# Optimization experiments

Hardware: AMD Instinct MI355X
Metric: run time of the kernel (lower is better)

Reference implementation:

```python
import jax, jax.numpy as jnp
import numpy as np

VOCAB, ATTR, B = 50257, 16, 256
EMB, ATTR_EMB, HID, ZDIM = 300, 200, 700, 500
MAXLEN = 30
SOS_IDX, EOS_IDX = 1, 2


def setup_inputs() -> dict:
    ks = jax.random.split(jax.random.key(0), 8)
    s = 0.02
    return {
        "z": jax.random.normal(ks[0], (B, ZDIM), jnp.float32),
        "l": jax.random.randint(ks[1], (B,), 0, ATTR),
        "emb_w": jax.random.normal(ks[2], (VOCAB, EMB), jnp.float32) * s,
        "attr_w": jax.random.normal(ks[3], (ATTR, ATTR_EMB), jnp.float32) * s,
        "W_ih": jax.random.normal(ks[4], (3 * HID, EMB), jnp.float32) * s,
        "W_hh": jax.random.normal(ks[5], (3 * HID, HID), jnp.float32) * s,
        "b_ih": jnp.zeros((3 * HID,), jnp.float32),
        "b_hh": jnp.zeros((3 * HID,), jnp.float32),
        "out_w": jax.random.normal(ks[6], (VOCAB, HID), jnp.float32) * s,
        "out_b": jnp.zeros((VOCAB,), jnp.float32),
    }


def gru_cell(x, h, W_ih, W_hh, b_ih, b_hh):
    # PyTorch GRU cell: r,z,n gate ordering
    gi = x @ W_ih.T + b_ih          # (B, 3H)
    gh = h @ W_hh.T + b_hh          # (B, 3H)
    i_r, i_z, i_n = jnp.split(gi, 3, axis=-1)
    h_r, h_z, h_n = jnp.split(gh, 3, axis=-1)
    r = jax.nn.sigmoid(i_r + h_r)
    zg = jax.nn.sigmoid(i_z + h_z)
    n = jnp.tanh(i_n + r * h_n)
    return (1.0 - zg) * n + zg * h


def reference(z, l, emb_w, attr_w, W_ih, W_hh, b_ih, b_hh, out_w, out_b):
    # hidden init: cat([z (B,500), attr_emb(l) (B,200)]) -> (B,700)
    h0 = jnp.concatenate([z, attr_w[l]], axis=-1)
    tok0 = jnp.full((B,), SOS_IDX, jnp.int32)
    keys = jax.random.split(jax.random.key(42), MAXLEN)

    def step(carry, k):
        h, tok = carry
        x = emb_w[tok]                                   # (B,300)
        h = gru_cell(x, h, W_ih, W_hh, b_ih, b_hh)       # (B,700)
        logits = h @ out_w.T + out_b                     # (B,VOCAB)
        # multinomial(softmax(logits), 1).detach()
        nxt = jax.lax.stop_gradient(
            jax.random.categorical(k, logits).astype(jnp.int32))
        return (h, nxt), (h, nxt)

    (h_last, _), (hy_t, y_t) = jax.lax.scan(step, (h0, tok0), keys)
    # final forced-EOS step
    eos = jnp.full((B,), EOS_IDX, jnp.int32)
    h_final = gru_cell(emb_w[eos], h_last, W_ih, W_hh, b_ih, b_hh)
    hy = jnp.concatenate([jnp.transpose(hy_t, (1, 0, 2)), h_final[:, None, :]], axis=1)  # (B,MAXLEN+1,700)
    y = jnp.concatenate([jnp.transpose(y_t, (1, 0)), eos[:, None]], axis=1)              # (B,MAXLEN+1)
    return hy, y
```

## Files before the change

kernel.cpp:

```cpp
#include <hip/hip_runtime.h>
#include <stdint.h>

#define VOCAB 50257
#define B 256
#define EMB 300
#define HID 700
#define G3 2100
#define ZDIM 500
#define ATTR_EMBD 200
#define MAXLEN 30
#define SEQ 31
#define HY_ELEMS (B*SEQ*HID)
#define KP 704
#define NKT 22
#define KIH 320
#define VPAD 50304
#define NVT 393
#define MPAD 2112
#define SOS_IDX 1
#define EOS_IDX 2
#define CHUNK 4096
#define TILE_STRIDE ((size_t)NKT * 2 * CHUNK)
#define NIT5 1572
#define NBLK5 1576

typedef _Float16 half8 __attribute__((ext_vector_type(8)));
typedef _Float16 half4 __attribute__((ext_vector_type(4)));
typedef float f32x4 __attribute__((ext_vector_type(4)));

typedef const __attribute__((address_space(1))) void* gas1_t;
typedef __attribute__((address_space(3))) void* las3_t;
__device__ __forceinline__ void gload_lds16(const void* g, void* l) {
  __builtin_amdgcn_global_load_lds((gas1_t)g, (las3_t)l, 16, 0, 0);
}

__device__ __forceinline__ uint32_t rotl32(uint32_t x, int r) {
  return (x << r) | (x >> (32 - r));
}

__device__ __forceinline__ void threefry2x32(uint32_t k0, uint32_t k1,
                                             uint32_t x0, uint32_t x1,
                                             uint32_t& o0, uint32_t& o1) {
  const uint32_t ks2 = k0 ^ k1 ^ 0x1BD11BDAu;
  x0 += k0; x1 += k1;
#define TF_R4(a, b, c, d)                                     \
  x0 += x1; x1 = rotl32(x1, a); x1 ^= x0;                     \
  x0 += x1; x1 = rotl32(x1, b); x1 ^= x0;                     \
  x0 += x1; x1 = rotl32(x1, c); x1 ^= x0;                     \
  x0 += x1; x1 = rotl32(x1, d); x1 ^= x0;
  TF_R4(13, 15, 26, 6)  x0 += k1;  x1 += ks2 + 1u;
  TF_R4(17, 29, 16, 24) x0 += ks2; x1 += k0 + 2u;
  TF_R4(13, 15, 26, 6)  x0 += k0;  x1 += k1 + 3u;
  TF_R4(17, 29, 16, 24) x0 += k1;  x1 += ks2 + 4u;
  TF_R4(13, 15, 26, 6)  x0 += ks2; x1 += k0 + 5u;
#undef TF_R4
  o0 = x0; o1 = x1;
}

__device__ __forceinline__ unsigned long long gumbel_pack(float s, uint32_t key0,
                                                          uint32_t key1, int b, int v) {
  uint32_t j = (uint32_t)(b * VOCAB + v);
  uint32_t o0, o1;
  threefry2x32(key0, key1, 0u, j, o0, o1);
  uint32_t bits = o0 ^ o1;
  float f = __uint_as_float((bits >> 9) | 0x3f800000u) - 1.0f;
  float u = fmaxf(f, 1.17549435e-38f);
  float g = -__logf(-__logf(u));
  s += g;
  uint32_t us = __float_as_uint(s);
  us = (us & 0x80000000u) ? ~us : (us | 0x80000000u);
  return ((unsigned long long)us << 32) | (uint32_t)(~(uint32_t)v);
}

struct hl16 { _Float16 hi, lo; };
__device__ __forceinline__ hl16 split16(float val, float scale) {
  float s = val * scale;
  _Float16 h = (_Float16)s;
  hl16 r;
  r.hi = h;
  r.lo = (_Float16)(s - (float)h);
  return r;
}

__global__ void k_init(const float* __restrict__ z, const int* __restrict__ l,
                       const float* __restrict__ attr_w, const float* __restrict__ emb_w,
                       float* __restrict__ hbuf0, uint32_t* __restrict__ keys,
                       unsigned long long* __restrict__ slots,
                       int* __restrict__ tok, float* __restrict__ y_out,
                       _Float16* __restrict__ h_hi, _Float16* __restrict__ h_lo,
                       _Float16* __restrict__ ht,
                       _Float16* __restrict__ x0_hi, _Float16* __restrict__ x0_lo,
                       _Float16* __restrict__ xe_hi, _Float16* __restrict__ xe_lo,
                       int full) {
  int idx = blockIdx.x * blockDim.x + threadIdx.x;
  if (idx < B * HID) {
    int b = idx / HID, i = idx % HID;
    float v = (i < ZDIM) ? z[b * ZDIM + i]
                         : attr_w[l[b] * ATTR_EMBD + (i - ZDIM)];
    hbuf0[idx] = v;
    hl16 r = split16(v, 8.0f);
    h_hi[b * KP + i] = r.hi;
    h_lo[b * KP + i] = r.lo;
  }
  if (idx < MAXLEN) {
    uint32_t o0, o1;
    threefry2x32(0u, 42u, 0u, (uint32_t)idx, o0, o1);
    keys[2 * idx] = o0; keys[2 * idx + 1] = o1;
  }
  if (idx < MAXLEN * B) slots[idx] = 0ull;
  if (idx < B) {
    tok[idx] = SOS_IDX;
    tok[31 * B + idx] = EOS_IDX;
    y_out[idx * SEQ + MAXLEN] = 2.0f;
  }
  if (idx < B * 4) {
    int b = idx >> 2, k = HID + (idx & 3);
    h_hi[b * KP + k] = (_Float16)0.0f;
    h_lo[b * KP + k] = (_Float16)0.0f;
    int c = b >> 7, row = b & 127, e = k & 7;
    size_t tb = (size_t)c * TILE_STRIDE + (size_t)21 * 2 * CHUNK
              + (3 * 128 + row) * 8 + e;
    ht[tb] = (_Float16)0.0f;
    ht[tb + CHUNK] = (_Float16)0.0f;
  }
  if (full && idx < KIH) {
    float v0 = (idx < EMB) ? emb_w[SOS_IDX * EMB + idx] : 0.0f;
    float ve = (idx < EMB) ? emb_w[EOS_IDX * EMB + idx] : 0.0f;
    hl16 r0 = split16(v0, 8.0f);
    hl16 re = split16(ve, 8.0f);
    for (int b = 0; b < B; ++b) {
      x0_hi[b * KIH + idx] = r0.hi; x0_lo[b * KIH + idx] = r0.lo;
      xe_hi[b * KIH + idx] = re.hi; xe_lo[b * KIH + idx] = re.lo;
    }
  }
}

__global__ void k_wsplit(const float* __restrict__ out_w, _Float16* __restrict__ wt) {
  size_t idx = (size_t)blockIdx.x * blockDim.x + threadIdx.x;
  if (idx >= (size_t)NVT * NKT * 1024) return;
  int h4 = (int)(idx & 1023);
  int ktp = (int)(idx >> 10);
  int kt = ktp % NKT, p = ktp / NKT;
  int slot4 = h4 >> 1, e0 = (h4 & 1) * 4;
  int kc = slot4 >> 7, row = slot4 & 127;
  int v = p * 128 + row;
  int k = kt * 32 + kc * 8 + e0;
  float x[4];
  if (v < VOCAB && k + 3 < HID) {
    const float4 xv = *(const float4*)&out_w[(size_t)v * HID + k];
    x[0] = xv.x; x[1] = xv.y; x[2] = xv.z; x[3] = xv.w;
  } else {
#pragma unroll
    for (int j = 0; j < 4; ++j)
      x[j] = (v < VOCAB && k + j < HID) ? out_w[(size_t)v * HID + k + j] : 0.0f;
  }
  half4 hi, lo;
#pragma unroll
  for (int j = 0; j < 4; ++j) {
    hl16 r = split16(x[j], 64.0f);
    hi[j] = r.hi; lo[j] = r.lo;
  }
  size_t base = (size_t)p * TILE_STRIDE + (size_t)kt * 2 * CHUNK + slot4 * 8 + e0;
  *(half4*)&wt[base] = hi;
  *(half4*)&wt[base + CHUNK] = lo;
}

__global__ void k_gwsplit(const float* __restrict__ src, _Float16* __restrict__ hi,
                          _Float16* __restrict__ lo, int Msrc, int Ksrc, int Kpad,
                          int tot4) {
  int idx = blockIdx.x * blockDim.x + threadIdx.x;
  if (idx >= tot4) return;
  size_t i4 = (size_t)idx * 4;
  int m = (int)(i4 / Kpad), k = (int)(i4 % Kpad);
  half4 h, l;
#pragma unroll
  for (int j = 0; j < 4; ++j) {
    float x = (m < Msrc && k + j < Ksrc) ? src[(size_t)m * Ksrc + k + j] : 0.0f;
    hl16 r = split16(x, 64.0f);
    h[j] = r.hi; l[j] = r.lo;
  }
  *(half4*)&hi[i4] = h;
  *(half4*)&lo[i4] = l;
}

__global__ __launch_bounds__(256, 4)
void k_gates2(const _Float16* __restrict__ wih_hi, const _Float16* __restrict__ wih_lo,
              const _Float16* __restrict__ whh_hi, const _Float16* __restrict__ whh_lo,
              const _Float16* __restrict__ x_hi, const _Float16* __restrict__ x_lo,
              const _Float16* __restrict__ h_hi, const _Float16* __restrict__ h_lo,
              float* __restrict__ gi, float* __restrict__ gh) {
  const int zz = blockIdx.z;
  const _Float16* __restrict__ Whi = zz ? whh_hi : wih_hi;
  const _Float16* __restrict__ Wlo = zz ? whh_lo : wih_lo;
  const _Float16* __restrict__ Xhi = zz ? h_hi : x_hi;
  const _Float16* __restrict__ Xlo = zz ? h_lo : x_lo;
  const int Kz = zz ? KP : KIH;
  float* __restrict__ out = zz ? gh : gi;

  const int jbase = blockIdx.x * 64;
  const int bbase = blockIdx.y * 64;
  __shared__ float4 lds[2][4][256];
  const int tid = threadIdx.x, lane = tid & 63, wid = tid >> 6;
  const int wj = wid >> 1, wb2 = wid & 1;
  const size_t wrow = (size_t)(jbase + lane) * Kz;
  const size_t xrow = (size_t)(bbase + lane) * Kz;

  f32x4 acc[2][2];
#pragma unroll
  for (int i = 0; i < 2; ++i)
#pragma unroll
    for (int j = 0; j < 2; ++j) acc[i][j] = (f32x4)0.0f;

#define GSTAGE(bf, k0)                                                   \
  {                                                                      \
    gload_lds16(Whi + wrow + (k0) + wid * 8, &lds[bf][0][wid * 64]);     \
    gload_lds16(Wlo + wrow + (k0) + wid * 8, &lds[bf][1][wid * 64]);     \
    gload_lds16(Xhi + xrow + (k0) + wid * 8, &lds[bf][2][wid * 64]);     \
    gload_lds16(Xlo + xrow + (k0) + wid * 8, &lds[bf][3][wid * 64]);     \
  }

  const int nt = Kz / 32;
  GSTAGE(0, 0)
  for (int kt = 0; kt < nt; ++kt) {
    const int cur = kt & 1;
    __syncthreads();
    if (kt + 1 < nt) GSTAGE(cur ^ 1, (kt + 1) * 32)
    const int kcf = (lane >> 4) * 64 + (lane & 15);
    half8 a_hi[2], a_lo[2];
#pragma unroll
    for (int fv = 0; fv < 2; ++fv) {
      int s = kcf + wj * 32 + fv * 16;
      a_hi[fv] = *(const half8*)&lds[cur][0][s];
      a_lo[fv] = *(const half8*)&lds[cur][1][s];
    }
#pragma unroll
    for (int fb = 0; fb < 2; ++fb) {
      int s = kcf + wb2 * 32 + fb * 16;
      half8 b_hi = *(const half8*)&lds[cur][2][s];
      half8 b_lo = *(const half8*)&lds[cur][3][s];
#pragma unroll
      for (int fv = 0; fv < 2; ++fv) {
        acc[fv][fb] = __builtin_amdgcn_mfma_f32_16x16x32_f16(a_hi[fv], b_hi,
                                                             acc[fv][fb], 0, 0, 0);
        acc[fv][fb] = __builtin_amdgcn_mfma_f32_16x16x32_f16(a_hi[fv], b_lo,
                                                             acc[fv][fb], 0, 0, 0);
        acc[fv][fb] = __builtin_amdgcn_mfma_f32_16x16x32_f16(a_lo[fv], b_hi,
                                                             acc[fv][fb], 0, 0, 0);
      }
    }
  }
#undef GSTAGE

  const float c2 = 1.0f / 512.0f;
#pragma unroll
  for (int fb = 0; fb < 2; ++fb) {
    const int b = bbase + wb2 * 32 + fb * 16 + (lane & 15);
#pragma unroll
    for (int fv = 0; fv < 2; ++fv) {
#pragma unroll
      for (int r = 0; r < 4; ++r) {
        int j = jbase + wj * 32 + fv * 16 + (lane >> 4) * 4 + r;
        if (j < G3) out[b * G3 + j] = acc[fv][fb][r] * c2;
      }
    }
  }
}

__global__ void k_gates(const float* __restrict__ W_ih, const float* __restrict__ W_hh,
                        const float* __restrict__ emb_w, const float* __restrict__ hprev,
                        const int* __restrict__ tok,
                        float* __restrict__ gi, float* __restrict__ gh) {
  const int zz = blockIdx.z;
  const float* __restrict__ W = zz ? W_hh : W_ih;
  const int K = zz ? HID : EMB;
  float* __restrict__ out = zz ? gh : gi;
  __shared__ float w_lds[20][36];
  __shared__ float xh_lds[20][36];
  const int jbase = blockIdx.x * 32;
  const int bbase = blockIdx.y * 32;
  const int tid = threadIdx.x;
  const int tj = tid % 16, tb = tid / 16;
  float a00 = 0.f, a01 = 0.f, a10 = 0.f, a11 = 0.f;
  for (int k0 = 0; k0 < K; k0 += 20) {
    for (int idx = tid; idx < 640; idx += 256) {
      int col = idx / 20, kk = idx % 20;
      int j = jbase + col;
      w_lds[kk][col] = (j < G3) ? W[j * K + k0 + kk] : 0.0f;
      int b = bbase + col;
      float xv;
      if (zz) xv = hprev[b * HID + k0 + kk];
      else    xv = emb_w[tok[b] * EMB + k0 + kk];
      xh_lds[kk][col] = xv;
    }
    __syncthreads();
#pragma unroll
    for (int kk = 0; kk < 20; ++kk) {
      float w0 = w_lds[kk][tj * 2], w1 = w_lds[kk][tj * 2 + 1];
      float h0 = xh_lds[kk][tb * 2], h1 = xh_lds[kk][tb * 2 + 1];
      a00 += w0 * h0; a01 += w0 * h1;
      a10 += w1 * h0; a11 += w1 * h1;
    }
    __syncthreads();
  }
  int j0 = jbase + tj * 2, b0 = bbase + tb * 2;
  if (j0 < G3)     { out[b0 * G3 + j0] = a00;     out[(b0 + 1) * G3 + j0] = a01; }
  if (j0 + 1 < G3) { out[b0 * G3 + j0 + 1] = a10; out[(b0 + 1) * G3 + j0 + 1] = a11; }
}

__global__ void k_hnew(const float* __restrict__ gi, const float* __restrict__ gh,
                       const float* __restrict__ b_ih, const float* __restrict__ b_hh,
                       const float* __restrict__ hprev, float* __restrict__ hnext,
                       float* __restrict__ hy, _Float16* __restrict__ h_hi,
                       _Float16* __restrict__ h_lo, _Float16* __restrict__ ht, int t) {
  int idx = blockIdx.x * blockDim.x + threadIdx.x;
  if (idx >= B * HID) return;
  int b = idx / HID, i = idx % HID;
  float ir = gi[b * G3 + i]            + b_ih[i];
  float iz = gi[b * G3 + HID + i]      + b_ih[HID + i];
  float in_ = gi[b * G3 + 2 * HID + i] + b_ih[2 * HID + i];
  float hr = gh[b * G3 + i]            + b_hh[i];
  float hz = gh[b * G3 + HID + i]      + b_hh[HID + i];
  float hn = gh[b * G3 + 2 * HID + i]  + b_hh[2 * HID + i];
  float r  = 1.0f / (1.0f + expf(-(ir + hr)));
  float zg = 1.0f / (1.0f + expf(-(iz + hz)));
  float n  = tanhf(in_ + r * hn);
  float h  = (1.0f - zg) * n + zg * hprev[idx];
  hnext[idx] = h;
  hy[(size_t)b * SEQ * HID + (size_t)t * HID + i] = h;
  hl16 rr = split16(h, 8.0f);
  h_hi[b * KP + i] = rr.hi;
  h_lo[b * KP + i] = rr.lo;
  int c = b >> 7, row = b & 127;
  size_t tb = (size_t)c * TILE_STRIDE + (size_t)(i >> 5) * 2 * CHUNK
            + ((((i >> 3) & 3) * 128 + row) * 8) + (i & 7);
  ht[tb] = rr.hi;
  ht[tb + CHUNK] = rr.lo;
}

__global__ __launch_bounds__(256, 3)
void k_logits7(const _Float16* __restrict__ wt, const _Float16* __restrict__ ht,
               const float* __restrict__ out_b, const uint32_t* __restrict__ keys,
               unsigned long long* __restrict__ slot, int t) {
  const int item = (blockIdx.x & 7) * 197 + (blockIdx.x >> 3);
  if (item >= NIT5) return;
  const int p = item >> 2, vh = (item >> 1) & 1, c = item & 1;

  __shared__ float4 ldsh[3][1024];
  const int tid = threadIdx.x, lane = tid & 63, wid = tid >> 6;
  const int wv = wid >> 1, wb = wid & 1;
  const int lq = lane >> 4, lr = lane & 15;

  const _Float16* __restrict__ wp = wt + (size_t)p * TILE_STRIDE;
  const _Float16* __restrict__ hp = ht + (size_t)c * TILE_STRIDE;

  const int wslot = lq * 128 + vh * 64 + wv * 32 + lr;
  const int hslot = lq * 128 + wb * 64 + lr;

  f32x4 acc[2][4];
#pragma unroll
  for (int i = 0; i < 2; ++i)
#pragma unroll
    for (int j = 0; j < 4; ++j) acc[i][j] = (f32x4)0.0f;

  half8 W0[4], W1[4], W2[4];

#define LOADW(W, ktv)                                                         \
  {                                                                           \
    const _Float16* bw = wp + (size_t)(ktv) * (2 * CHUNK);                    \
    _Pragma("unroll")                                                         \
    for (int fv = 0; fv < 2; ++fv) {                                          \
      W[fv * 2 + 0] = *(const half8*)(bw + (wslot + fv * 16) * 8);            \
      W[fv * 2 + 1] = *(const half8*)(bw + CHUNK + (wslot + fv * 16) * 8);    \
    }                                                                         \
  }
#define STAGEH(bf, ktv)                                                       \
  {                                                                           \
    const _Float16* bh = hp + (size_t)(ktv) * (2 * CHUNK);                    \
    _Pragma("unroll")                                                         \
    for (int j = 0; j < 4; ++j)                                               \
      gload_lds16(bh + (j * 256 + wid * 64 + lane) * 8,                       \
                  &ldsh[bf][j * 256 + wid * 64]);                             \
  }
#define MFMAB(W, BF)                                                          \
  _Pragma("unroll")                                                           \
  for (int fb = 0; fb < 4; ++fb) {                                            \
    half8 hhi = *(const half8*)&ldsh[BF][hslot + fb * 16];                    \
    half8 hlo = *(const half8*)&ldsh[BF][512 + hslot + fb * 16];              \
    _Pragma("unroll")                                                         \
    for (int fv = 0; fv < 2; ++fv) {                                          \
      acc[fv][fb] = __builtin_amdgcn_mfma_f32_16x16x32_f16(                   \
          W[fv * 2 + 0], hhi, acc[fv][fb], 0, 0, 0);                          \
      acc[fv][fb] = __builtin_amdgcn_mfma_f32_16x16x32_f16(                   \
          W[fv * 2 + 0], hlo, acc[fv][fb], 0, 0, 0);                          \
      acc[fv][fb] = __builtin_amdgcn_mfma_f32_16x16x32_f16(                   \
          W[fv * 2 + 1], hhi, acc[fv][fb], 0, 0, 0);                          \
    }                                                                         \
  }
#define STEP(ktv, BC, BP, WCUR, WNEW)                                         \
  {                                                                           \
    asm volatile("s_waitcnt vmcnt(4)" ::: "memory");                          \
    __builtin_amdgcn_sched_barrier(0);                                        \
    __builtin_amdgcn_s_barrier();                                             \
    __builtin_amdgcn_sched_barrier(0);                                        \
    if ((ktv) + 2 < NKT) {                                                    \
      STAGEH(BP, (ktv) + 2)                                                   \
      LOADW(WNEW, (ktv) + 2)                                                  \
    }                                                                         \
    __builtin_amdgcn_s_setprio(1);                                            \
    MFMAB(WCUR, BC)                                                           \
    __builtin_amdgcn_s_setprio(0);                                            \
  }

  STAGEH(0, 0)
  STAGEH(1, 1)
  LOADW(W0, 0)
  LOADW(W1, 1)
#pragma unroll 1
  for (int base = 0; base < 21; base += 3) {
    STEP(base + 0, 0, 2, W0, W2)
    STEP(base + 1, 1, 0, W1, W0)
    STEP(base + 2, 2, 1, W2, W1)
  }
  STEP(21, 0, 2, W0, W2)
#undef STEP
#undef LOADW
#undef STAGEH
#undef MFMAB

  const uint32_t key0 = keys[2 * t], key1 = keys[2 * t + 1];
  const float c2 = 1.0f / 512.0f;
  const int vbase0 = p * 128 + vh * 64 + wv * 32;
#pragma unroll
  for (int fb = 0; fb < 4; ++fb) {
    const int b = c * 128 + wb * 64 + fb * 16 + lr;
    unsigned long long best = 0ull;
#pragma unroll
    for (int fv = 0; fv < 2; ++fv) {
#pragma unroll
      for (int r = 0; r < 4; ++r) {
        int v = vbase0 + fv * 16 + lq * 4 + r;
        if (v < VOCAB) {
          float s = acc[fv][fb][r] * c2 + out_b[v];
          unsigned long long cand = gumbel_pack(s, key0, key1, b, v);
          if (cand > best) best = cand;
        }
      }
    }
    unsigned long long o;
    o = __shfl_xor(best, 16, 64); if (o > best) best = o;
    o = __shfl_xor(best, 32, 64); if (o > best) best = o;
    if (lq == 0) atomicMax(&slot[b], best);
  }
}

#define WPITCH 68
#define HPITCH 260
__global__ __launch_bounds__(256)
void k_logits_f32(const float* __restrict__ h, const float* __restrict__ out_w,
                  const float* __restrict__ out_b, const uint32_t* __restrict__ keys,
                  unsigned long long* __restrict__ slot, int t) {
  __shared__ float w_lds[20][WPITCH];
  __shared__ float h_lds[20][HPITCH];
  const int vbase = blockIdx.x * 64;
  const int tid = threadIdx.x;
  const int tv = tid % 8, tb = tid / 8;
  float acc[8][8];
#pragma unroll
  for (int i = 0; i < 8; ++i)
#pragma unroll
    for (int j = 0; j < 8; ++j) acc[i][j] = 0.f;

  for (int k0 = 0; k0 < HID; k0 += 20) {
    for (int idx = tid; idx < 64 * 20; idx += 256) {
      int vv = idx / 20, kk = idx % 20;
      int v = vbase + vv;
      w_lds[kk][vv] = (v < VOCAB) ? out_w[(size_t)v * HID + k0 + kk] : 0.0f;
    }
    for (int idx = tid; idx < 256 * 20; idx += 256) {
      int bb = idx / 20, kk = idx % 20;
      h_lds[kk][bb] = h[bb * HID + k0 + kk];
    }
    __syncthreads();
#pragma unroll
    for (int kk = 0; kk < 20; ++kk) {
      float wv[8], hv[8];
      *(float4*)&wv[0] = *(const float4*)&w_lds[kk][tv * 8];
      *(float4*)&wv[4] = *(const float4*)&w_lds[kk][tv * 8 + 4];
      *(float4*)&hv[0] = *(const float4*)&h_lds[kk][tb * 8];
      *(float4*)&hv[4] = *(const float4*)&h_lds[kk][tb * 8 + 4];
#pragma unroll
      for (int iv = 0; iv < 8; ++iv)
#pragma unroll
        for (int ib = 0; ib < 8; ++ib) acc[iv][ib] += wv[iv] * hv[ib];
    }
    __syncthreads();
  }

  const uint32_t key0 = keys[2 * t], key1 = keys[2 * t + 1];
#pragma unroll
  for (int ib = 0; ib < 8; ++ib) {
    const int b = tb * 8 + ib;
    unsigned long long best = 0ull;
#pragma unroll
    for (int iv = 0; iv < 8; ++iv) {
      int v = vbase + tv * 8 + iv;
      if (v >= VOCAB) continue;
      unsigned long long cand = gumbel_pack(acc[iv][ib] + out_b[v], key0, key1, b, v);
      if (cand > best) best = cand;
    }
#pragma unroll
    for (int off = 1; off < 8; off <<= 1) {
      unsigned long long other = __shfl_xor(best, off, 64);
      if (other > best) best = other;
    }
    if (tv == 0) atomicMax(&slot[b], best);
  }
}

__global__ void k_tok2(const unsigned long long* __restrict__ slot,
                       const float* __restrict__ emb_w,
                       int* __restrict__ tok_next, float* __restrict__ y_out,
                       _Float16* __restrict__ xc_hi, _Float16* __restrict__ xc_lo,
                       int t, int full) {
  const int b = blockIdx.x;
  const int c = threadIdx.x;
  unsigned long long p = slot[b];
  uint32_t v = ~((uint32_t)(p & 0xFFFFFFFFull));
  if (c == 0) {
    tok_next[b] = (int)v;
    y_out[b * SEQ + t] = (float)v;
  }
  if (!full) return;
  if (c < 75) {
    float4 xv = *(const float4*)&emb_w[(size_t)v * EMB + c * 4];
    half4 hi, lo;
    hl16 r0 = split16(xv.x, 8.0f); hi[0] = r0.hi; lo[0] = r0.lo;
    hl16 r1 = split16(xv.y, 8.0f); hi[1] = r1.hi; lo[1] = r1.lo;
    hl16 r2 = split16(xv.z, 8.0f); hi[2] = r2.hi; lo[2] = r2.lo;
    hl16 r3 = split16(xv.w, 8.0f); hi[3] = r3.hi; lo[3] = r3.lo;
    *(half4*)&xc_hi[b * KIH + c * 4] = hi;
    *(half4*)&xc_lo[b * KIH + c * 4] = lo;
  } else if (c < 80) {
    *(half4*)&xc_hi[b * KIH + c * 4] = (half4)(_Float16)0.0f;
    *(half4*)&xc_lo[b * KIH + c * 4] = (half4)(_Float16)0.0f;
  }
}

extern "C" void kernel_launch(void* const* d_in, const int* in_sizes, int n_in,
                              void* d_out, int out_size, void* d_ws, size_t ws_size,
                              hipStream_t stream) {
  const float* z      = (const float*)d_in[0];
  const int*   l      = (const int*)  d_in[1];
  const float* emb_w  = (const float*)d_in[2];
  const float* attr_w = (const float*)d_in[3];
  const float* W_ih   = (const float*)d_in[4];
  const float* W_hh   = (const float*)d_in[5];
  const float* b_ih   = (const float*)d_in[6];
  const float* b_hh   = (const float*)d_in[7];
  const float* out_w  = (const float*)d_in[8];
  const float* out_b  = (const float*)d_in[9];

  float* hy    = (float*)d_out;
  float* y_out = (float*)d_out + HY_ELEMS;

  char* ws = (char*)d_ws;
  size_t off = 0;
  uint32_t* keys            = (uint32_t*)(ws + off);           off += 256;
  unsigned long long* slots = (unsigned long long*)(ws + off); off += (size_t)MAXLEN * B * 8;
  int* tokbuf               = (int*)(ws + off);                off += (size_t)32 * B * 4;
  float* hbuf               = (float*)(ws + off);              off += (size_t)2 * B * HID * 4;
  float* gi                 = (float*)(ws + off);              off += (size_t)B * G3 * 4;
  float* gh                 = (float*)(ws + off);              off += (size_t)B * G3 * 4;
  _Float16* h_hi            = (_Float16*)(ws + off);           off += (size_t)B * KP * 2;
  _Float16* h_lo            = (_Float16*)(ws + off);           off += (size_t)B * KP * 2;
  _Float16* ht              = (_Float16*)(ws + off);           off += (size_t)2 * TILE_STRIDE * 2;
  _Float16* wt              = (_Float16*)(ws + off);           off += (size_t)NVT * TILE_STRIDE * 2;
  const size_t tier1_end = off;
  _Float16* wih_hi          = (_Float16*)(ws + off);           off += (size_t)MPAD * KIH * 2;
  _Float16* wih_lo          = (_Float16*)(ws + off);           off += (size_t)MPAD * KIH * 2;
  _Float16* whh_hi          = (_Float16*)(ws + off);           off += (size_t)MPAD * KP * 2;
  _Float16* whh_lo          = (_Float16*)(ws + off);           off += (size_t)MPAD * KP * 2;
  _Float16* x0_hi           = (_Float16*)(ws + off);           off += (size_t)B * KIH * 2;
  _Float16* x0_lo           = (_Float16*)(ws + off);           off += (size_t)B * KIH * 2;
  _Float16* xe_hi           = (_Float16*)(ws + off);           off += (size_t)B * KIH * 2;
  _Float16* xe_lo           = (_Float16*)(ws + off);           off += (size_t)B * KIH * 2;
  _Float16* xc_hi           = (_Float16*)(ws + off);           off += (size_t)B * KIH * 2;
  _Float16* xc_lo           = (_Float16*)(ws + off);           off += (size_t)B * KIH * 2;
  const size_t tier2_end = off;
  const int tier = (ws_size >= tier2_end) ? 2 : ((ws_size >= tier1_end) ? 1 : 0);

  k_init<<<(B * HID + 255) / 256, 256, 0, stream>>>(
      z, l, attr_w, emb_w, hbuf, keys, slots, tokbuf, y_out, h_hi, h_lo, ht,
      x0_hi, x0_lo, xe_hi, xe_lo, (tier == 2) ? 1 : 0);

  if (tier >= 1) {
    size_t tot = (size_t)NVT * NKT * 1024;
    k_wsplit<<<(int)((tot + 255) / 256), 256, 0, stream>>>(out_w, wt);
  }
  if (tier == 2) {
    int tih = MPAD * KIH / 4, thh = MPAD * KP / 4;
    k_gwsplit<<<(tih + 255) / 256, 256, 0, stream>>>(W_ih, wih_hi, wih_lo, G3, EMB, KIH, tih);
    k_gwsplit<<<(thh + 255) / 256, 256, 0, stream>>>(W_hh, whh_hi, whh_lo, G3, HID, KP, thh);
  }

  for (int t = 0; t <= MAXLEN; ++t) {
    float* hprev = hbuf + (t % 2) * B * HID;
    float* hnext = hbuf + ((t + 1) % 2) * B * HID;

    if (tier == 2) {
      const _Float16* xh = (t == 0) ? x0_hi : ((t == MAXLEN) ? xe_hi : xc_hi);
      const _Float16* xl = (t == 0) ? x0_lo : ((t == MAXLEN) ? xe_lo : xc_lo);
      dim3 g2(33, 4, 2);
      k_gates2<<<g2, 256, 0, stream>>>(wih_hi, wih_lo, whh_hi, whh_lo,
                                       xh, xl, h_hi, h_lo, gi, gh);
    } else {
      const int* tok_t = tokbuf + ((t == MAXLEN) ? 31 : t) * B;
      dim3 ggrid(66, 8, 2);
      k_gates<<<ggrid, 256, 0, stream>>>(W_ih, W_hh, emb_w, hprev, tok_t, gi, gh);
    }
    k_hnew<<<(B * HID + 255) / 256, 256, 0, stream>>>(gi, gh, b_ih, b_hh, hprev,
                                                      hnext, hy, h_hi, h_lo, ht, t);
    if (t < MAXLEN) {
      if (tier >= 1) {
        k_logits7<<<NBLK5, 256, 0, stream>>>(wt, ht, out_b, keys,
                                             slots + (size_t)t * B, t);
      } else {
        k_logits_f32<<<(VOCAB + 63) / 64, 256, 0, stream>>>(hnext, out_w, out_b, keys,
                                                            slots + (size_t)t * B, t);
      }
      k_tok2<<<B, 128, 0, stream>>>(slots + (size_t)t * B, emb_w,
                                    tokbuf + (t + 1) * B, y_out, xc_hi, xc_lo,
                                    t, (tier == 2) ? 1 : 0);
    }
  }
}
```

Before: 3.739 ms.

## Interleave Gumbel noise generation with MFMA K-loop in logits kernel

The logits kernel now computes the threefry-based Gumbel noise (plus bias) for each output element during the K-loop, right after each step's MFMA batch, instead of in the epilogue. The goal is to hide the integer and transcendental work behind memory latency and matrix ops. The loop is fully unrolled to schedule these slots, 32 noise values are held in registers, and the occupancy hint drops from 3 to 2 blocks per CU. The higher register pressure and lower occupancy could cut latency hiding for the global and LDS loads.

```diff
diff --git a/kernel.cpp b/kernel.cpp
--- a/kernel.cpp
+++ b/kernel.cpp
@@ -337,8 +337,8 @@
   ht[tb + CHUNK] = rr.lo;
 }
 
-__global__ __launch_bounds__(256, 3)
-void k_logits7(const _Float16* __restrict__ wt, const _Float16* __restrict__ ht,
+__global__ __launch_bounds__(256, 2)
+void k_logits8(const _Float16* __restrict__ wt, const _Float16* __restrict__ ht,
                const float* __restrict__ out_b, const uint32_t* __restrict__ keys,
                unsigned long long* __restrict__ slot, int t) {
   const int item = (blockIdx.x & 7) * 197 + (blockIdx.x >> 3);
@@ -355,6 +355,18 @@
 
   const int wslot = lq * 128 + vh * 64 + wv * 32 + lr;
   const int hslot = lq * 128 + wb * 64 + lr;
+  const int vbase0 = p * 128 + vh * 64 + wv * 32;
+  const int bbase0 = c * 128 + wb * 64 + lr;
+  const uint32_t key0 = keys[2 * t], key1 = keys[2 * t + 1];
+
+  float ob[8];
+#pragma unroll
+  for (int fv = 0; fv < 2; ++fv)
+#pragma unroll
+    for (int r = 0; r < 4; ++r) {
+      int v = vbase0 + fv * 16 + lq * 4 + r;
+      ob[fv * 4 + r] = (v < VOCAB) ? out_b[v] : 0.0f;
+    }
 
   f32x4 acc[2][4];
 #pragma unroll
@@ -362,6 +374,7 @@
 #pragma unroll
     for (int j = 0; j < 4; ++j) acc[i][j] = (f32x4)0.0f;
 
+  float q[32];
   half8 W0[4], W1[4], W2[4];
 
 #define LOADW(W, ktv)                                                         \
@@ -396,7 +409,19 @@
           W[fv * 2 + 1], hhi, acc[fv][fb], 0, 0, 0);                          \
     }                                                                         \
   }
-#define STEP(ktv, BC, BP, WCUR, WNEW)                                         \
+#define QS(s)                                                                 \
+  if ((s) < 32) {                                                             \
+    const int fb_ = (s) >> 3, fv_ = ((s) >> 2) & 1, r_ = (s) & 3;             \
+    const int b_ = bbase0 + fb_ * 16;                                         \
+    const int v_ = vbase0 + fv_ * 16 + lq * 4 + r_;                           \
+    uint32_t o0_, o1_;                                                        \
+    threefry2x32(key0, key1, 0u, (uint32_t)(b_ * VOCAB + v_), o0_, o1_);      \
+    uint32_t bits_ = o0_ ^ o1_;                                               \
+    float f_ = __uint_as_float((bits_ >> 9) | 0x3f800000u) - 1.0f;            \
+    float u_ = fmaxf(f_, 1.17549435e-38f);                                    \
+    q[(s)] = ob[fv_ * 4 + r_] - __logf(-__logf(u_));                          \
+  }
+#define STEP(ktv, BC, BP, WCUR, WNEW, S0, S1)                                 \
   {                                                                           \
     asm volatile("s_waitcnt vmcnt(4)" ::: "memory");                          \
     __builtin_amdgcn_sched_barrier(0);                                        \
@@ -409,30 +434,46 @@
     __builtin_amdgcn_s_setprio(1);                                            \
     MFMAB(WCUR, BC)                                                           \
     __builtin_amdgcn_s_setprio(0);                                            \
+    QS(S0)                                                                    \
+    QS(S1)                                                                    \
   }
 
   STAGEH(0, 0)
   STAGEH(1, 1)
   LOADW(W0, 0)
   LOADW(W1, 1)
-#pragma unroll 1
-  for (int base = 0; base < 21; base += 3) {
-    STEP(base + 0, 0, 2, W0, W2)
-    STEP(base + 1, 1, 0, W1, W0)
-    STEP(base + 2, 2, 1, W2, W1)
-  }
-  STEP(21, 0, 2, W0, W2)
+  STEP(0, 0, 2, W0, W2, 0, 1)
+  STEP(1, 1, 0, W1, W0, 2, 3)
+  STEP(2, 2, 1, W2, W1, 4, 5)
+  STEP(3, 0, 2, W0, W2, 6, 7)
+  STEP(4, 1, 0, W1, W0, 8, 9)
+  STEP(5, 2, 1, W2, W1, 10, 11)
+  STEP(6, 0, 2, W0, W2, 12, 13)
+  STEP(7, 1, 0, W1, W0, 14, 15)
+  STEP(8, 2, 1, W2, W1, 16, 17)
+  STEP(9, 0, 2, W0, W2, 18, 19)
+  STEP(10, 1, 0, W1, W0, 20, 32)
+  STEP(11, 2, 1, W2, W1, 21, 32)
+  STEP(12, 0, 2, W0, W2, 22, 32)
+  STEP(13, 1, 0, W1, W0, 23, 32)
+  STEP(14, 2, 1, W2, W1, 24, 32)
+  STEP(15, 0, 2, W0, W2, 25, 32)
+  STEP(16, 1, 0, W1, W0, 26, 32)
+  STEP(17, 2, 1, W2, W1, 27, 32)
+  STEP(18, 0, 2, W0, W2, 28, 32)
+  STEP(19, 1, 0, W1, W0, 29, 32)
+  STEP(20, 2, 1, W2, W1, 30, 32)
+  STEP(21, 0, 2, W0, W2, 31, 32)
 #undef STEP
+#undef QS
 #undef LOADW
 #undef STAGEH
 #undef MFMAB
 
-  const uint32_t key0 = keys[2 * t], key1 = keys[2 * t + 1];
   const float c2 = 1.0f / 512.0f;
-  const int vbase0 = p * 128 + vh * 64 + wv * 32;
 #pragma unroll
   for (int fb = 0; fb < 4; ++fb) {
-    const int b = c * 128 + wb * 64 + fb * 16 + lr;
+    const int b = bbase0 + fb * 16;
     unsigned long long best = 0ull;
 #pragma unroll
     for (int fv = 0; fv < 2; ++fv) {
@@ -440,8 +481,11 @@
       for (int r = 0; r < 4; ++r) {
         int v = vbase0 + fv * 16 + lq * 4 + r;
         if (v < VOCAB) {
-          float s = acc[fv][fb][r] * c2 + out_b[v];
-          unsigned long long cand = gumbel_pack(s, key0, key1, b, v);
+          float sc = acc[fv][fb][r] * c2 + q[fb * 8 + fv * 4 + r];
+          uint32_t us = __float_as_uint(sc);
+          us = (us & 0x80000000u) ? ~us : (us | 0x80000000u);
+          unsigned long long cand =
+              ((unsigned long long)us << 32) | (uint32_t)(~(uint32_t)v);
           if (cand > best) best = cand;
         }
       }
@@ -622,7 +666,7 @@
                                                       hnext, hy, h_hi, h_lo, ht, t);
     if (t < MAXLEN) {
       if (tier >= 1) {
-        k_logits7<<<NBLK5, 256, 0, stream>>>(wt, ht, out_b, keys,
+        k_logits8<<<NBLK5, 256, 0, stream>>>(wt, ht, out_b, keys,
                                              slots + (size_t)t * B, t);
       } else {
         k_logits_f32<<<(VOCAB + 63) / 64, 256, 0, stream>>>(hnext, out_w, out_b, keys,
```

Result: faster. 3.623 ms (-3.1%).
